# Kernel optimization log

Measured on AMD Instinct MI355X. Metric: run time of the kernel, lower is better.

Reference implementation:

```python
import jax, jax.numpy as jnp
import numpy as np

N_HEADS = 8

def _rotate_half(x):
    # interleaved pairs: (x1, x2) -> (-x2, x1), rotary_embedding_torch style
    x = x.reshape(*x.shape[:-1], -1, 2)
    x1, x2 = x[..., 0], x[..., 1]
    return jnp.stack([-x2, x1], axis=-1).reshape(*x.shape[:-2], -1)

def _apply_rotary(freqs, t):
    # freqs: (seq, d), t: (..., seq, d)
    return t * jnp.cos(freqs) + _rotate_half(t) * jnp.sin(freqs)

def _sdpa(q, k, v):
    # q,k,v: (b, g, h, s, d) ; attention over s
    d = q.shape[-1]
    scores = jnp.einsum('bghqd,bghkd->bghqk', q, k) / jnp.sqrt(jnp.asarray(d, q.dtype))
    w = jax.nn.softmax(scores, axis=-1)
    return jnp.einsum('bghqk,bghkd->bghqd', w, v)

def setup_inputs() -> dict:
    key = jax.random.key(0)
    ks = jax.random.split(key, 5)
    B, T, Fd, D = 4, 256, 64, 256
    x = jax.random.normal(ks[0], (B, T, Fd, D), dtype=jnp.float32)
    W_attn = jax.random.normal(ks[1], (D, 5 * D), dtype=jnp.float32) * 0.02
    W_proj = jax.random.normal(ks[2], (D, D), dtype=jnp.float32) * 0.02
    hd = D // N_HEADS
    rotary_t = jax.random.uniform(ks[3], (T, hd), dtype=jnp.float32) * 2 * np.pi
    rotary_f = jax.random.uniform(ks[4], (Fd, hd), dtype=jnp.float32) * 2 * np.pi
    return {"x": x, "W_attn": W_attn, "W_proj": W_proj,
            "rotary_t": rotary_t, "rotary_f": rotary_f}

def reference(x, W_attn, W_proj, rotary_t, rotary_f):
    B, T, Fd, D = x.shape
    h = N_HEADS
    d = D // h
    # fused QKV: (B,T,F,5D) -> (5, B, h, T, F, d)
    qkv = (x @ W_attn).reshape(B, T, Fd, 5, h, d).transpose(3, 0, 4, 1, 2, 5)
    q_t, q_f, k_t, k_f, v = qkv[0], qkv[1], qkv[2], qkv[3], qkv[4]
    # ---- time attention: batch over (b, f), attend over t ----
    # b h t f d -> b f h t d
    q_t = jnp.transpose(q_t, (0, 3, 1, 2, 4))
    k_t = jnp.transpose(k_t, (0, 3, 1, 2, 4))
    v_t = jnp.transpose(v, (0, 3, 1, 2, 4))
    q_t = _apply_rotary(rotary_t, q_t)
    k_t = _apply_rotary(rotary_t, k_t)
    v_t = _sdpa(q_t, k_t, v_t)  # (b, f, h, t, d)
    # ---- frequency attention: batch over (b, t), attend over f ----
    # b h t f d -> b t h f d
    q_f = jnp.transpose(q_f, (0, 2, 1, 3, 4))
    k_f = jnp.transpose(k_f, (0, 2, 1, 3, 4))
    # b f h t d -> b t h f d
    v_f = jnp.transpose(v_t, (0, 3, 2, 1, 4))
    q_f = _apply_rotary(rotary_f, q_f)
    k_f = _apply_rotary(rotary_f, k_f)
    y = _sdpa(q_f, k_f, v_f)  # (b, t, h, f, d)
    # b t h f d -> b t f (h d)
    y = jnp.transpose(y, (0, 1, 3, 2, 4)).reshape(B, T, Fd, D)
    return y @ W_proj
```

## Files before the change

### kernel.cpp

```cpp
#include <hip/hip_runtime.h>

typedef unsigned short u16;
typedef unsigned int u32;
typedef short s16x8 __attribute__((ext_vector_type(8)));
typedef u16 u16x4 __attribute__((ext_vector_type(4)));
typedef float f32x4 __attribute__((ext_vector_type(4)));
typedef u32 u32x2 __attribute__((ext_vector_type(2)));
typedef u32 u32x4 __attribute__((ext_vector_type(4)));

#define MFMA(a,b,c) __builtin_amdgcn_mfma_f32_16x16x32_bf16((a),(b),(c),0,0,0)

static const size_t PL = 16777216;

__device__ __forceinline__ float b2f(u16 b) {
    return __uint_as_float(((unsigned int)b) << 16);
}
__device__ __forceinline__ u16 f2b(float f) {
    unsigned int u = __float_as_uint(f);
    unsigned int r = (u + 0x7FFFu + ((u >> 16) & 1u)) >> 16;
    return (u16)r;
}
__device__ __forceinline__ u32 cvtpk(float lo, float hi) {
    u32 r;
    asm("v_cvt_pk_bf16_f32 %0, %1, %2" : "=v"(r) : "v"(lo), "v"(hi));
    return r;
}
__device__ __forceinline__ float fexp2(float x) {
#if __has_builtin(__builtin_amdgcn_exp2f)
    return __builtin_amdgcn_exp2f(x);
#else
    return exp2f(x);
#endif
}

__device__ __forceinline__ s16x8 rot8(const u16* __restrict__ src,
                                      const float* __restrict__ cp,
                                      const float* __restrict__ sp) {
    s16x8 u = *(const s16x8*)src;
    f32x4 c0 = *(const f32x4*)cp, c1 = *(const f32x4*)(cp + 4);
    f32x4 s0 = *(const f32x4*)sp, s1 = *(const f32x4*)(sp + 4);
    float x[8];
#pragma unroll
    for (int j = 0; j < 8; j++) x[j] = b2f((u16)u[j]);
    float c[8] = {c0[0], c0[1], c0[2], c0[3], c1[0], c1[1], c1[2], c1[3]};
    float s[8] = {s0[0], s0[1], s0[2], s0[3], s1[0], s1[1], s1[2], s1[3]};
    u32x4 r;
#pragma unroll
    for (int p = 0; p < 4; p++) {
        float e = x[2 * p], o = x[2 * p + 1];
        float lo = e * c[2 * p] - o * s[2 * p];
        float hi = fmaf(e, s[2 * p + 1], o * c[2 * p + 1]);
        r[p] = cvtpk(lo, hi);
    }
    return __builtin_bit_cast(s16x8, r);
}

__global__ void prep_aux_k(const float* __restrict__ Wa, const float* __restrict__ Wp,
                           const float* __restrict__ rt, const float* __restrict__ rf,
                           u16* __restrict__ wt_a, u16* __restrict__ wt_p,
                           float* __restrict__ ct_t, float* __restrict__ st_t,
                           float* __restrict__ ct_f, float* __restrict__ st_f) {
    int i = blockIdx.x * 256 + threadIdx.x;
    if (i < 81920) {
        int idx = i * 4;
        int k = idx / 1280, n = idx - k * 1280;
        f32x4 v = *(const f32x4*)&Wa[idx];
#pragma unroll
        for (int j = 0; j < 4; j++) wt_a[(n + j) * 256 + k] = f2b(v[j]);
    } else if (i < 98304) {
        int idx = (i - 81920) * 4;
        int k = idx >> 8, n = idx & 255;
        f32x4 v = *(const f32x4*)&Wp[idx];
#pragma unroll
        for (int j = 0; j < 4; j++) wt_p[(n + j) * 256 + k] = f2b(v[j]);
    } else if (i < 100352) {
        int j = (i - 98304) * 4;
        f32x4 v = *(const f32x4*)&rt[j];
        f32x4 c, s;
#pragma unroll
        for (int jj = 0; jj < 4; jj++) { float ss, cc; __sincosf(v[jj], &ss, &cc); c[jj] = cc; s[jj] = ss; }
        *(f32x4*)&ct_t[j] = c; *(f32x4*)&st_t[j] = s;
    } else if (i < 100864) {
        int j = (i - 100352) * 4;
        f32x4 v = *(const f32x4*)&rf[j];
        f32x4 c, s;
#pragma unroll
        for (int jj = 0; jj < 4; jj++) { float ss, cc; __sincosf(v[jj], &ss, &cc); c[jj] = cc; s[jj] = ss; }
        *(f32x4*)&ct_f[j] = c; *(f32x4*)&st_f[j] = s;
    }
}

template<int NT, bool AF32, bool TO_PLANES>
__global__ __launch_bounds__(256, 2) void gemm_k(const void* __restrict__ Ap,
                                                 const u16* __restrict__ Bt,
                                                 u16* __restrict__ outp,
                                                 float* __restrict__ outf) {
    __shared__ __align__(16) u16 As[2][128][40];
    __shared__ __align__(16) u16 Bs[2][128][40];
    const float* Af = (const float*)Ap;
    const u16* Ab = (const u16*)Ap;
    int bid = blockIdx.x;
    int xcd = bid & 7, slot = bid >> 3;
    int L = xcd * ((512 * NT) / 8) + slot;
    int mt = L / NT, nt = L - mt * NT;
    int m0 = mt * 128, n0 = nt * 128;
    int tid = threadIdx.x, lane = tid & 63, w = tid >> 6;
    int wm = w >> 1, wn = w & 1;
    int g = lane >> 4, lr = lane & 15;
    f32x4 acc[4][4] = {};
    f32x4 apf[4]; s16x8 apb[2]; s16x8 bpf[2];

    auto loadA = [&](int k0) {
        if (AF32) {
#pragma unroll
            for (int i = 0; i < 4; i++) {
                int c = tid + i * 256, row = c >> 3, c4 = (c & 7) * 4;
                apf[i] = *(const f32x4*)&Af[(size_t)(m0 + row) * 256 + k0 + c4];
            }
        } else {
#pragma unroll
            for (int i = 0; i < 2; i++) {
                int c = tid + i * 256, row = c >> 2, p = c & 3;
                apb[i] = *(const s16x8*)&Ab[(size_t)(m0 + row) * 256 + k0 + p * 8];
            }
        }
    };
    auto loadB = [&](int k0) {
#pragma unroll
        for (int i = 0; i < 2; i++) {
            int c = tid + i * 256, row = c >> 2, p = c & 3;
            bpf[i] = *(const s16x8*)&Bt[(size_t)(n0 + row) * 256 + k0 + p * 8];
        }
    };
    auto storeAB = [&](int buf) {
        if (AF32) {
#pragma unroll
            for (int i = 0; i < 4; i++) {
                int c = tid + i * 256, row = c >> 3, c4 = (c & 7) * 4;
                u32x2 pk = { cvtpk(apf[i][0], apf[i][1]), cvtpk(apf[i][2], apf[i][3]) };
                *(u32x2*)&As[buf][row][c4] = pk;
            }
        } else {
#pragma unroll
            for (int i = 0; i < 2; i++) {
                int c = tid + i * 256, row = c >> 2, p = c & 3;
                *(s16x8*)&As[buf][row][p * 8] = apb[i];
            }
        }
#pragma unroll
        for (int i = 0; i < 2; i++) {
            int c = tid + i * 256, row = c >> 2, p = c & 3;
            *(s16x8*)&Bs[buf][row][p * 8] = bpf[i];
        }
    };

    loadA(0); loadB(0);
    storeAB(0);
    loadA(32); loadB(32);
    __syncthreads();

    for (int s = 0; s < 8; s++) {
        int cur = s & 1;
        s16x8 af[4], bf[4];
#pragma unroll
        for (int mi = 0; mi < 4; mi++) af[mi] = *(const s16x8*)&As[cur][wm * 64 + mi * 16 + lr][g * 8];
#pragma unroll
        for (int ni = 0; ni < 4; ni++) bf[ni] = *(const s16x8*)&Bs[cur][wn * 64 + ni * 16 + lr][g * 8];
        if (s < 7) storeAB(cur ^ 1);
        if (s < 6) { loadA((s + 2) * 32); loadB((s + 2) * 32); }
#pragma unroll
        for (int ni = 0; ni < 4; ni++)
#pragma unroll
            for (int mi = 0; mi < 4; mi++)
                acc[ni][mi] = MFMA(bf[ni], af[mi], acc[ni][mi]);
        __syncthreads();
    }

#pragma unroll
    for (int ni = 0; ni < 4; ni++) {
#pragma unroll
        for (int mi = 0; mi < 4; mi++) {
            int token = m0 + wm * 64 + mi * 16 + lr;
            int n = n0 + wn * 64 + ni * 16 + g * 4;
            if (TO_PLANES) {
                u32x2 pk = { cvtpk(acc[ni][mi][0], acc[ni][mi][1]),
                             cvtpk(acc[ni][mi][2], acc[ni][mi][3]) };
                int pl = n >> 8, c = n & 255, h = c >> 5, d0 = c & 31;
                int b = token >> 14, t = (token >> 6) & 255, f = token & 63;
                size_t addr = (pl == 1 || pl == 3)
                    ? ((size_t)(((b * 256 + t) * 8 + h) * 64 + f) * 32 + d0)
                    : ((size_t)(((b * 64 + f) * 8 + h) * 256 + t) * 32 + d0);
                *(u32x2*)&outp[(size_t)pl * PL + addr] = pk;
            } else {
                *(f32x4*)&outf[(size_t)token * 256 + n] = acc[ni][mi];
            }
        }
    }
}

__global__ __launch_bounds__(256, 3) void attn_time_k(const u16* __restrict__ qt,
                                                      const u16* __restrict__ kt,
                                                      const u16* __restrict__ vp,
                                                      u16* __restrict__ y1,
                                                      const float* __restrict__ ct,
                                                      const float* __restrict__ st) {
    __shared__ __align__(16) u16 K_l[256][40];
    __shared__ __align__(16) u16 Vt[32][264];
    __shared__ __align__(16) u16 Pst[4][2][16][40];
    int bid = blockIdx.x;
    int xcd = bid & 7, slot = bid >> 3;
    int L = xcd * 512 + slot;
    int qh = L & 1, head = L >> 1;
    int h = head & 7, f = (head >> 3) & 63, b = head >> 9;
    int tid = threadIdx.x, lane = tid & 63, w = tid >> 6;
    int g = lane >> 4, lr = lane & 15;
    const u16* Khead = kt + (size_t)head * 8192;
    const u16* Qhead = qt + (size_t)head * 8192;
    const u16* Vhead = vp + (size_t)head * 8192;

#pragma unroll
    for (int i = 0; i < 4; i++) {
        int c = tid + i * 256;
        int t = c >> 2, p = (c & 3) * 8;
        *(s16x8*)&K_l[t][p] = rot8(Khead + t * 32 + p, ct + t * 32 + p, st + t * 32 + p);
    }
    {
        int ka = (tid & 63) * 4, db = (tid >> 6) * 8;
        const u16* vb = Vhead + (size_t)ka * 32 + db;
        s16x8 r0 = *(const s16x8*)(vb);
        s16x8 r1 = *(const s16x8*)(vb + 32);
        s16x8 r2 = *(const s16x8*)(vb + 64);
        s16x8 r3 = *(const s16x8*)(vb + 96);
#pragma unroll
        for (int dd = 0; dd < 8; dd++) {
            u16x4 pk = { (u16)r0[dd], (u16)r1[dd], (u16)r2[dd], (u16)r3[dd] };
            *(u16x4*)&Vt[db + dd][ka] = pk;
        }
    }
    int qbase = qh * 128 + w * 32;
    s16x8 qf_[2];
#pragma unroll
    for (int qi = 0; qi < 2; qi++) {
        int q = qbase + qi * 16 + lr;
        qf_[qi] = rot8(Qhead + q * 32 + g * 8, ct + q * 32 + g * 8, st + q * 32 + g * 8);
    }
    __syncthreads();

    f32x4 sT[16][2] = {};
#pragma unroll
    for (int ki = 0; ki < 16; ki++) {
        s16x8 kf8 = *(const s16x8*)&K_l[ki * 16 + lr][g * 8];
        sT[ki][0] = MFMA(kf8, qf_[0], sT[ki][0]);
        sT[ki][1] = MFMA(kf8, qf_[1], sT[ki][1]);
    }
    const float sc2 = 0.17677669529663687f * 1.4426950408889634f;
    float rsum[2];
#pragma unroll
    for (int qi = 0; qi < 2; qi++) {
        float m = -1e30f;
#pragma unroll
        for (int ki = 0; ki < 16; ki++)
#pragma unroll
            for (int r = 0; r < 4; r++) m = fmaxf(m, sT[ki][qi][r]);
        m = fmaxf(m, __shfl_xor(m, 16));
        m = fmaxf(m, __shfl_xor(m, 32));
        float msc = m * sc2;
        float ssum = 0.f;
#pragma unroll
        for (int ki = 0; ki < 16; ki++)
#pragma unroll
            for (int r = 0; r < 4; r++) {
                float p = fexp2(sT[ki][qi][r] * sc2 - msc);
                sT[ki][qi][r] = p; ssum += p;
            }
        ssum += __shfl_xor(ssum, 16);
        ssum += __shfl_xor(ssum, 32);
        rsum[qi] = 1.0f / ssum;
    }

    f32x4 o_[2][2] = {};
#pragma unroll
    for (int ks = 0; ks < 8; ks++) {
        s16x8 vf0 = *(const s16x8*)&Vt[lr][ks * 32 + g * 8];
        s16x8 vf1 = *(const s16x8*)&Vt[16 + lr][ks * 32 + g * 8];
#pragma unroll
        for (int qi = 0; qi < 2; qi++) {
            u32x2 w0 = { cvtpk(sT[2 * ks][qi][0], sT[2 * ks][qi][1]),
                         cvtpk(sT[2 * ks][qi][2], sT[2 * ks][qi][3]) };
            u32x2 w1 = { cvtpk(sT[2 * ks + 1][qi][0], sT[2 * ks + 1][qi][1]),
                         cvtpk(sT[2 * ks + 1][qi][2], sT[2 * ks + 1][qi][3]) };
            *(u32x2*)&Pst[w][qi][lr][g * 4] = w0;
            *(u32x2*)&Pst[w][qi][lr][16 + g * 4] = w1;
            s16x8 pf = *(const s16x8*)&Pst[w][qi][lr][g * 8];
            o_[0][qi] = MFMA(vf0, pf, o_[0][qi]);
            o_[1][qi] = MFMA(vf1, pf, o_[1][qi]);
        }
    }
#pragma unroll
    for (int qi = 0; qi < 2; qi++) {
        int q = qbase + qi * 16 + lr;
        float rs = rsum[qi];
        u16* dst = y1 + ((size_t)(((b * 256 + q) * 8 + h) * 64 + f)) * 32;
#pragma unroll
        for (int di = 0; di < 2; di++) {
            u32x2 ob = { cvtpk(o_[di][qi][0] * rs, o_[di][qi][1] * rs),
                         cvtpk(o_[di][qi][2] * rs, o_[di][qi][3] * rs) };
            *(u32x2*)&dst[di * 16 + g * 4] = ob;
        }
    }
}

__global__ __launch_bounds__(256, 2) void attn_freq_k(const u16* __restrict__ qfp,
                                                      const u16* __restrict__ kfp,
                                                      const u16* __restrict__ y1,
                                                      u16* __restrict__ y2,
                                                      const float* __restrict__ ct,
                                                      const float* __restrict__ st) {
    __shared__ __align__(16) u16 K_l[4][64][40];
    __shared__ __align__(16) u16 Vt[4][32][72];
    __shared__ __align__(16) u16 Pst[4][2][16][40];
    int tid = threadIdx.x, lane = tid & 63, w = tid >> 6;
    int g = lane >> 4, lr = lane & 15;
    int head = blockIdx.x * 4 + w;
    int h = head & 7, t = (head >> 3) & 255, b = head >> 11;
    const u16* Khead = kfp + (size_t)head * 2048;
    const u16* Qhead = qfp + (size_t)head * 2048;
    const u16* Vhead = y1 + (size_t)head * 2048;

#pragma unroll
    for (int i = 0; i < 4; i++) {
        int c = i * 64 + lane;
        int row = c >> 2, p = (c & 3) * 8;
        *(s16x8*)&K_l[w][row][p] = rot8(Khead + row * 32 + p, ct + row * 32 + p, st + row * 32 + p);
    }
    {
        int ka = lr * 4, db = g * 8;
        const u16* vb = Vhead + (size_t)ka * 32 + db;
        s16x8 r0 = *(const s16x8*)(vb);
        s16x8 r1 = *(const s16x8*)(vb + 32);
        s16x8 r2 = *(const s16x8*)(vb + 64);
        s16x8 r3 = *(const s16x8*)(vb + 96);
#pragma unroll
        for (int dd = 0; dd < 8; dd++) {
            u16x4 pk = { (u16)r0[dd], (u16)r1[dd], (u16)r2[dd], (u16)r3[dd] };
            *(u16x4*)&Vt[w][db + dd][ka] = pk;
        }
    }
    s16x8 qfr[4];
#pragma unroll
    for (int qi = 0; qi < 4; qi++) {
        int q = qi * 16 + lr;
        qfr[qi] = rot8(Qhead + q * 32 + g * 8, ct + q * 32 + g * 8, st + q * 32 + g * 8);
    }

    f32x4 sT[4][4] = {};
#pragma unroll
    for (int ki = 0; ki < 4; ki++) {
        s16x8 kf8 = *(const s16x8*)&K_l[w][ki * 16 + lr][g * 8];
#pragma unroll
        for (int qi = 0; qi < 4; qi++) sT[ki][qi] = MFMA(kf8, qfr[qi], sT[ki][qi]);
    }
    const float sc2 = 0.17677669529663687f * 1.4426950408889634f;
    float rsum[4];
#pragma unroll
    for (int qi = 0; qi < 4; qi++) {
        float m = -1e30f;
#pragma unroll
        for (int ki = 0; ki < 4; ki++)
#pragma unroll
            for (int r = 0; r < 4; r++) m = fmaxf(m, sT[ki][qi][r]);
        m = fmaxf(m, __shfl_xor(m, 16));
        m = fmaxf(m, __shfl_xor(m, 32));
        float msc = m * sc2;
        float ssum = 0.f;
#pragma unroll
        for (int ki = 0; ki < 4; ki++)
#pragma unroll
            for (int r = 0; r < 4; r++) {
                float p = fexp2(sT[ki][qi][r] * sc2 - msc);
                sT[ki][qi][r] = p; ssum += p;
            }
        ssum += __shfl_xor(ssum, 16);
        ssum += __shfl_xor(ssum, 32);
        rsum[qi] = 1.0f / ssum;
    }

    f32x4 o_[2][4] = {};
#pragma unroll
    for (int ks = 0; ks < 2; ks++) {
        s16x8 vf0 = *(const s16x8*)&Vt[w][lr][ks * 32 + g * 8];
        s16x8 vf1 = *(const s16x8*)&Vt[w][16 + lr][ks * 32 + g * 8];
#pragma unroll
        for (int qi = 0; qi < 4; qi++) {
            u32x2 w0 = { cvtpk(sT[2 * ks][qi][0], sT[2 * ks][qi][1]),
                         cvtpk(sT[2 * ks][qi][2], sT[2 * ks][qi][3]) };
            u32x2 w1 = { cvtpk(sT[2 * ks + 1][qi][0], sT[2 * ks + 1][qi][1]),
                         cvtpk(sT[2 * ks + 1][qi][2], sT[2 * ks + 1][qi][3]) };
            *(u32x2*)&Pst[w][qi & 1][lr][g * 4] = w0;
            *(u32x2*)&Pst[w][qi & 1][lr][16 + g * 4] = w1;
            s16x8 pf = *(const s16x8*)&Pst[w][qi & 1][lr][g * 8];
            o_[0][qi] = MFMA(vf0, pf, o_[0][qi]);
            o_[1][qi] = MFMA(vf1, pf, o_[1][qi]);
        }
    }
#pragma unroll
    for (int qi = 0; qi < 4; qi++) {
        int q = qi * 16 + lr;
        float rs = rsum[qi];
        u16* dst = y2 + ((size_t)((b * 256 + t) * 64 + q)) * 256 + h * 32;
#pragma unroll
        for (int di = 0; di < 2; di++) {
            u32x2 ob = { cvtpk(o_[di][qi][0] * rs, o_[di][qi][1] * rs),
                         cvtpk(o_[di][qi][2] * rs, o_[di][qi][3] * rs) };
            *(u32x2*)&dst[di * 16 + g * 4] = ob;
        }
    }
}

extern "C" void kernel_launch(void* const* d_in, const int* in_sizes, int n_in,
                              void* d_out, int out_size, void* d_ws, size_t ws_size,
                              hipStream_t stream) {
    const float* x  = (const float*)d_in[0];
    const float* Wa = (const float*)d_in[1];
    const float* Wp = (const float*)d_in[2];
    const float* rt = (const float*)d_in[3];
    const float* rf = (const float*)d_in[4];
    float* out = (float*)d_out;

    u16* planes = (u16*)d_ws;
    u16* qt  = planes;
    u16* qfp = planes + PL;
    u16* ktp = planes + 2 * PL;
    u16* kfp = planes + 3 * PL;
    u16* vp  = planes + 4 * PL;
    u16* y1  = planes + 5 * PL;
    u16* y2  = ktp;
    float* ct_t = (float*)(planes + 6 * PL);
    float* st_t = ct_t + 8192;
    float* ct_f = st_t + 8192;
    float* st_f = ct_f + 2048;
    u16* wt_a = (u16*)(st_f + 2048);
    u16* wt_p = wt_a + 327680;

    prep_aux_k<<<394, 256, 0, stream>>>(Wa, Wp, rt, rf, wt_a, wt_p, ct_t, st_t, ct_f, st_f);
    gemm_k<10, true, true><<<5120, 256, 0, stream>>>(x, wt_a, planes, nullptr);
    attn_time_k<<<4096, 256, 0, stream>>>(qt, ktp, vp, y1, ct_t, st_t);
    attn_freq_k<<<2048, 256, 0, stream>>>(qfp, kfp, y1, y2, ct_f, st_f);
    gemm_k<2, false, false><<<1024, 256, 0, stream>>>(y2, wt_p, nullptr, out);
}
```

Before: 239.2 us.

## Make QKV GEMM persistent with cross-tile prefetch pipeline

Turns the GEMM into a persistent-style kernel where each block processes T output tiles back to back. Loads for the next tile are issued while the current tile's last k-steps and epilogue run, and the QKV GEMM launches 1024 blocks with 5 tiles each instead of 5120 blocks. Launch bounds rise from 2 to 4 waves-per-EU hints, which may pressure registers. The aim is to hide per-tile prologue and epilogue latency, at the cost of fewer blocks and a possible load imbalance.

After: 411.2 us. 1.72x slower.

```diff
diff --git a/kernel.cpp b/kernel.cpp
--- a/kernel.cpp
+++ b/kernel.cpp
@@ -90,8 +90,8 @@
     }
 }
 
-template<int NT, bool AF32, bool TO_PLANES>
-__global__ __launch_bounds__(256, 2) void gemm_k(const void* __restrict__ Ap,
+template<int NT, int T, bool AF32, bool TO_PLANES>
+__global__ __launch_bounds__(256, 4) void gemm_k(const void* __restrict__ Ap,
                                                  const u16* __restrict__ Bt,
                                                  u16* __restrict__ outp,
                                                  float* __restrict__ outf) {
@@ -99,18 +99,24 @@
     __shared__ __align__(16) u16 Bs[2][128][40];
     const float* Af = (const float*)Ap;
     const u16* Ab = (const u16*)Ap;
+    constexpr int U = T * 8;
+    constexpr int CPX = (512 * NT) / 8;
     int bid = blockIdx.x;
     int xcd = bid & 7, slot = bid >> 3;
-    int L = xcd * ((512 * NT) / 8) + slot;
-    int mt = L / NT, nt = L - mt * NT;
-    int m0 = mt * 128, n0 = nt * 128;
     int tid = threadIdx.x, lane = tid & 63, w = tid >> 6;
     int wm = w >> 1, wn = w & 1;
     int g = lane >> 4, lr = lane & 15;
     f32x4 acc[4][4] = {};
     f32x4 apf[4]; s16x8 apb[2]; s16x8 bpf[2];
 
-    auto loadA = [&](int k0) {
+    auto coords = [&](int tau, int& m0, int& n0) {
+        int L = xcd * CPX + tau * 128 + slot;
+        int mt = L / NT, nt = L - mt * NT;
+        m0 = mt * 128; n0 = nt * 128;
+    };
+    auto issueLoads = [&](int u) {
+        int tau = u >> 3, k0 = (u & 7) * 32;
+        int m0, n0; coords(tau, m0, n0);
         if (AF32) {
 #pragma unroll
             for (int i = 0; i < 4; i++) {
@@ -124,8 +130,6 @@
                 apb[i] = *(const s16x8*)&Ab[(size_t)(m0 + row) * 256 + k0 + p * 8];
             }
         }
-    };
-    auto loadB = [&](int k0) {
 #pragma unroll
         for (int i = 0; i < 2; i++) {
             int c = tid + i * 256, row = c >> 2, p = c & 3;
@@ -153,48 +157,53 @@
             *(s16x8*)&Bs[buf][row][p * 8] = bpf[i];
         }
     };
-
-    loadA(0); loadB(0);
+    auto epilogue = [&](int tau) {
+        int m0, n0; coords(tau, m0, n0);
+#pragma unroll
+        for (int ni = 0; ni < 4; ni++) {
+#pragma unroll
+            for (int mi = 0; mi < 4; mi++) {
+                int token = m0 + wm * 64 + mi * 16 + lr;
+                int n = n0 + wn * 64 + ni * 16 + g * 4;
+                if (TO_PLANES) {
+                    u32x2 pk = { cvtpk(acc[ni][mi][0], acc[ni][mi][1]),
+                                 cvtpk(acc[ni][mi][2], acc[ni][mi][3]) };
+                    int pl = n >> 8, c = n & 255, h = c >> 5, d0 = c & 31;
+                    int b = token >> 14, t = (token >> 6) & 255, f = token & 63;
+                    size_t addr = (pl == 1 || pl == 3)
+                        ? ((size_t)(((b * 256 + t) * 8 + h) * 64 + f) * 32 + d0)
+                        : ((size_t)(((b * 64 + f) * 8 + h) * 256 + t) * 32 + d0);
+                    *(u32x2*)&outp[(size_t)pl * PL + addr] = pk;
+                } else {
+                    *(f32x4*)&outf[(size_t)token * 256 + n] = acc[ni][mi];
+                }
+                acc[ni][mi] = f32x4{0.f, 0.f, 0.f, 0.f};
+            }
+        }
+    };
+
+    issueLoads(0);
     storeAB(0);
-    loadA(32); loadB(32);
+    issueLoads(1);
     __syncthreads();
 
-    for (int s = 0; s < 8; s++) {
-        int cur = s & 1;
+#pragma unroll 2
+    for (int u = 0; u < U; u++) {
+        int cur = u & 1;
         s16x8 af[4], bf[4];
 #pragma unroll
         for (int mi = 0; mi < 4; mi++) af[mi] = *(const s16x8*)&As[cur][wm * 64 + mi * 16 + lr][g * 8];
 #pragma unroll
         for (int ni = 0; ni < 4; ni++) bf[ni] = *(const s16x8*)&Bs[cur][wn * 64 + ni * 16 + lr][g * 8];
-        if (s < 7) storeAB(cur ^ 1);
-        if (s < 6) { loadA((s + 2) * 32); loadB((s + 2) * 32); }
+        if (u + 1 < U) storeAB(cur ^ 1);
+        if (u + 2 < U) issueLoads(u + 2);
 #pragma unroll
         for (int ni = 0; ni < 4; ni++)
 #pragma unroll
             for (int mi = 0; mi < 4; mi++)
                 acc[ni][mi] = MFMA(bf[ni], af[mi], acc[ni][mi]);
+        if ((u & 7) == 7) epilogue(u >> 3);
         __syncthreads();
-    }
-
-#pragma unroll
-    for (int ni = 0; ni < 4; ni++) {
-#pragma unroll
-        for (int mi = 0; mi < 4; mi++) {
-            int token = m0 + wm * 64 + mi * 16 + lr;
-            int n = n0 + wn * 64 + ni * 16 + g * 4;
-            if (TO_PLANES) {
-                u32x2 pk = { cvtpk(acc[ni][mi][0], acc[ni][mi][1]),
-                             cvtpk(acc[ni][mi][2], acc[ni][mi][3]) };
-                int pl = n >> 8, c = n & 255, h = c >> 5, d0 = c & 31;
-                int b = token >> 14, t = (token >> 6) & 255, f = token & 63;
-                size_t addr = (pl == 1 || pl == 3)
-                    ? ((size_t)(((b * 256 + t) * 8 + h) * 64 + f) * 32 + d0)
-                    : ((size_t)(((b * 64 + f) * 8 + h) * 256 + t) * 32 + d0);
-                *(u32x2*)&outp[(size_t)pl * PL + addr] = pk;
-            } else {
-                *(f32x4*)&outf[(size_t)token * 256 + n] = acc[ni][mi];
-            }
-        }
     }
 }
 
@@ -443,8 +452,8 @@
     u16* wt_p = wt_a + 327680;
 
     prep_aux_k<<<394, 256, 0, stream>>>(Wa, Wp, rt, rf, wt_a, wt_p, ct_t, st_t, ct_f, st_f);
-    gemm_k<10, true, true><<<5120, 256, 0, stream>>>(x, wt_a, planes, nullptr);
+    gemm_k<10, 5, true, true><<<1024, 256, 0, stream>>>(x, wt_a, planes, nullptr);
     attn_time_k<<<4096, 256, 0, stream>>>(qt, ktp, vp, y1, ct_t, st_t);
     attn_freq_k<<<2048, 256, 0, stream>>>(qfp, kfp, y1, y2, ct_f, st_f);
-    gemm_k<2, false, false><<<1024, 256, 0, stream>>>(y2, wt_p, nullptr, out);
-}
+    gemm_k<2, 1, false, false><<<1024, 256, 0, stream>>>(y2, wt_p, nullptr, out);
+}
```

## Pre-convert x to bf16 in separate pass and widen GEMM K-tile to 64

Applied to the files above, without the earlier changes.

Adds a standalone kernel that converts the fp32 input x to bf16 into workspace (reusing the y1 buffer), so the QKV GEMM always loads bf16 A tiles instead of fp32 with in-loop conversion. The GEMM K-step grows from 32 to 64 with larger padded LDS tiles, halving the number of barrier/pipeline iterations. This costs an extra full read of x plus a write and reread of the bf16 copy, plus more LDS per block, which may reduce occupancy.

New measurement: 211.5 us. 1.13x faster.

```diff
diff --git a/kernel.cpp b/kernel.cpp
--- a/kernel.cpp
+++ b/kernel.cpp
@@ -53,6 +53,14 @@
         r[p] = cvtpk(lo, hi);
     }
     return __builtin_bit_cast(s16x8, r);
+}
+
+__global__ void prep_x_k(const float* __restrict__ x, u16* __restrict__ xb) {
+    size_t i = ((size_t)blockIdx.x * 256 + threadIdx.x) * 8;
+    f32x4 a = *(const f32x4*)(x + i);
+    f32x4 b = *(const f32x4*)(x + i + 4);
+    u32x4 o = { cvtpk(a[0], a[1]), cvtpk(a[2], a[3]), cvtpk(b[0], b[1]), cvtpk(b[2], b[3]) };
+    *(u32x4*)(xb + i) = o;
 }
 
 __global__ void prep_aux_k(const float* __restrict__ Wa, const float* __restrict__ Wp,
@@ -90,15 +98,13 @@
     }
 }
 
-template<int NT, bool AF32, bool TO_PLANES>
-__global__ __launch_bounds__(256, 2) void gemm_k(const void* __restrict__ Ap,
+template<int NT, bool TO_PLANES>
+__global__ __launch_bounds__(256, 2) void gemm_k(const u16* __restrict__ A,
                                                  const u16* __restrict__ Bt,
                                                  u16* __restrict__ outp,
                                                  float* __restrict__ outf) {
-    __shared__ __align__(16) u16 As[2][128][40];
-    __shared__ __align__(16) u16 Bs[2][128][40];
-    const float* Af = (const float*)Ap;
-    const u16* Ab = (const u16*)Ap;
+    __shared__ __align__(16) u16 As[2][128][72];
+    __shared__ __align__(16) u16 Bs[2][128][72];
     int bid = blockIdx.x;
     int xcd = bid & 7, slot = bid >> 3;
     int L = xcd * ((512 * NT) / 8) + slot;
@@ -108,71 +114,54 @@
     int wm = w >> 1, wn = w & 1;
     int g = lane >> 4, lr = lane & 15;
     f32x4 acc[4][4] = {};
-    f32x4 apf[4]; s16x8 apb[2]; s16x8 bpf[2];
-
-    auto loadA = [&](int k0) {
-        if (AF32) {
-#pragma unroll
-            for (int i = 0; i < 4; i++) {
-                int c = tid + i * 256, row = c >> 3, c4 = (c & 7) * 4;
-                apf[i] = *(const f32x4*)&Af[(size_t)(m0 + row) * 256 + k0 + c4];
-            }
-        } else {
-#pragma unroll
-            for (int i = 0; i < 2; i++) {
-                int c = tid + i * 256, row = c >> 2, p = c & 3;
-                apb[i] = *(const s16x8*)&Ab[(size_t)(m0 + row) * 256 + k0 + p * 8];
-            }
-        }
-    };
-    auto loadB = [&](int k0) {
-#pragma unroll
-        for (int i = 0; i < 2; i++) {
-            int c = tid + i * 256, row = c >> 2, p = c & 3;
-            bpf[i] = *(const s16x8*)&Bt[(size_t)(n0 + row) * 256 + k0 + p * 8];
+    s16x8 apb[4], bpb[4];
+
+    auto loadAB = [&](int k0) {
+#pragma unroll
+        for (int i = 0; i < 4; i++) {
+            int c = tid + i * 256, row = c >> 3, p = (c & 7) * 8;
+            apb[i] = *(const s16x8*)&A[(size_t)(m0 + row) * 256 + k0 + p];
+            bpb[i] = *(const s16x8*)&Bt[(size_t)(n0 + row) * 256 + k0 + p];
         }
     };
     auto storeAB = [&](int buf) {
-        if (AF32) {
-#pragma unroll
-            for (int i = 0; i < 4; i++) {
-                int c = tid + i * 256, row = c >> 3, c4 = (c & 7) * 4;
-                u32x2 pk = { cvtpk(apf[i][0], apf[i][1]), cvtpk(apf[i][2], apf[i][3]) };
-                *(u32x2*)&As[buf][row][c4] = pk;
-            }
-        } else {
-#pragma unroll
-            for (int i = 0; i < 2; i++) {
-                int c = tid + i * 256, row = c >> 2, p = c & 3;
-                *(s16x8*)&As[buf][row][p * 8] = apb[i];
-            }
-        }
-#pragma unroll
-        for (int i = 0; i < 2; i++) {
-            int c = tid + i * 256, row = c >> 2, p = c & 3;
-            *(s16x8*)&Bs[buf][row][p * 8] = bpf[i];
+#pragma unroll
+        for (int i = 0; i < 4; i++) {
+            int c = tid + i * 256, row = c >> 3, p = (c & 7) * 8;
+            *(s16x8*)&As[buf][row][p] = apb[i];
+            *(s16x8*)&Bs[buf][row][p] = bpb[i];
         }
     };
 
-    loadA(0); loadB(0);
+    loadAB(0);
     storeAB(0);
-    loadA(32); loadB(32);
+    loadAB(64);
     __syncthreads();
 
-    for (int s = 0; s < 8; s++) {
+    for (int s = 0; s < 4; s++) {
         int cur = s & 1;
-        s16x8 af[4], bf[4];
-#pragma unroll
-        for (int mi = 0; mi < 4; mi++) af[mi] = *(const s16x8*)&As[cur][wm * 64 + mi * 16 + lr][g * 8];
-#pragma unroll
-        for (int ni = 0; ni < 4; ni++) bf[ni] = *(const s16x8*)&Bs[cur][wn * 64 + ni * 16 + lr][g * 8];
-        if (s < 7) storeAB(cur ^ 1);
-        if (s < 6) { loadA((s + 2) * 32); loadB((s + 2) * 32); }
+        s16x8 af0[4], bf0[4];
+#pragma unroll
+        for (int mi = 0; mi < 4; mi++) af0[mi] = *(const s16x8*)&As[cur][wm * 64 + mi * 16 + lr][g * 8];
+#pragma unroll
+        for (int ni = 0; ni < 4; ni++) bf0[ni] = *(const s16x8*)&Bs[cur][wn * 64 + ni * 16 + lr][g * 8];
+        if (s < 3) storeAB(cur ^ 1);
+        if (s < 2) loadAB((s + 2) * 64);
 #pragma unroll
         for (int ni = 0; ni < 4; ni++)
 #pragma unroll
             for (int mi = 0; mi < 4; mi++)
-                acc[ni][mi] = MFMA(bf[ni], af[mi], acc[ni][mi]);
+                acc[ni][mi] = MFMA(bf0[ni], af0[mi], acc[ni][mi]);
+        s16x8 af1[4], bf1[4];
+#pragma unroll
+        for (int mi = 0; mi < 4; mi++) af1[mi] = *(const s16x8*)&As[cur][wm * 64 + mi * 16 + lr][32 + g * 8];
+#pragma unroll
+        for (int ni = 0; ni < 4; ni++) bf1[ni] = *(const s16x8*)&Bs[cur][wn * 64 + ni * 16 + lr][32 + g * 8];
+#pragma unroll
+        for (int ni = 0; ni < 4; ni++)
+#pragma unroll
+            for (int mi = 0; mi < 4; mi++)
+                acc[ni][mi] = MFMA(bf1[ni], af1[mi], acc[ni][mi]);
         __syncthreads();
     }
 
@@ -434,6 +423,7 @@
     u16* kfp = planes + 3 * PL;
     u16* vp  = planes + 4 * PL;
     u16* y1  = planes + 5 * PL;
+    u16* xb  = y1;
     u16* y2  = ktp;
     float* ct_t = (float*)(planes + 6 * PL);
     float* st_t = ct_t + 8192;
@@ -442,9 +432,10 @@
     u16* wt_a = (u16*)(st_f + 2048);
     u16* wt_p = wt_a + 327680;
 
+    prep_x_k<<<8192, 256, 0, stream>>>(x, xb);
     prep_aux_k<<<394, 256, 0, stream>>>(Wa, Wp, rt, rf, wt_a, wt_p, ct_t, st_t, ct_f, st_f);
-    gemm_k<10, true, true><<<5120, 256, 0, stream>>>(x, wt_a, planes, nullptr);
+    gemm_k<10, true><<<5120, 256, 0, stream>>>(xb, wt_a, planes, nullptr);
     attn_time_k<<<4096, 256, 0, stream>>>(qt, ktp, vp, y1, ct_t, st_t);
     attn_freq_k<<<2048, 256, 0, stream>>>(qfp, kfp, y1, y2, ct_f, st_f);
-    gemm_k<2, false, false><<<1024, 256, 0, stream>>>(y2, wt_p, nullptr, out);
-}
+    gemm_k<2, false><<<1024, 256, 0, stream>>>(y2, wt_p, nullptr, out);
+}
```
